# Kernel optimization log

Measured on AMD Instinct MI355X. Metric: run time of the kernel, lower is better.

## Reference

```python
import jax, jax.numpy as jnp
import numpy as np

K = 4096   # infeatures (k)
N = 4096   # outfeatures (n)
G = 128    # quantization groupsize
M = 8192   # tokens (batch*seq)


def setup_inputs() -> dict:
    key = jax.random.key(0)
    kA, kB, kS = jax.random.split(key, 3)
    A = jax.random.normal(kA, (M, K), dtype=jnp.float32)
    # Packed int4 weights: each int32 holds 8 consecutive nibbles along k.
    B = jax.random.randint(kB, (K // 8, N), 0, 2**31 - 1, dtype=jnp.int32)
    # Per-group symmetric scales, positive and small like real quant scales.
    s = jax.random.uniform(kS, (K // G, N), dtype=jnp.float32) * 0.02 + 0.005
    return {"A": A, "B": B, "s": s}


def dequant(B, s):
    """Unpack int4 nibbles, center by 8 (symmetric zero-point), apply per-group scales.
    B: (K//8, N) int32 -> returns (K, N) float weight matrix."""
    shifts = (jnp.arange(8, dtype=jnp.int32) * 4)
    nib = (B[:, None, :] >> shifts[None, :, None]) & 0xF       # (K//8, 8, N) in [0,15]
    w = nib.reshape(B.shape[0] * 8, B.shape[1]).astype(s.dtype) - 8.0  # (K, N)
    scale = jnp.repeat(s, w.shape[0] // s.shape[0], axis=0)    # (K, N) group-broadcast
    return w * scale


def reference(A, B, s):
    # C = A @ dequant(B, s): fused int4-dequant GEMM (Marlin forward math).
    return A @ dequant(B, s)
```

## Files before the change

kernel.cpp:

```cpp
#include <hip/hip_runtime.h>
#include <hip/hip_fp16.h>


constexpr int MDIM = 8192;
constexpr int NDIM = 4096;
constexpr int KDIM = 4096;
constexpr int BM = 128;
constexpr int BN = 128;
constexpr int BK = 64;
constexpr int THREADS = 256;
constexpr int KSTEPS = KDIM / BK;
constexpr int TILE_B = BM * BK * 2;
constexpr int MT = MDIM / BM;
constexpr int NT = NDIM / BN;
constexpr size_t AH_BYTES = (size_t)MT * KSTEPS * TILE_B;
constexpr size_t WT_BYTES = (size_t)NT * KSTEPS * TILE_B;

typedef _Float16 f16x8 __attribute__((ext_vector_type(8)));
typedef float f32x4 __attribute__((ext_vector_type(4)));
typedef __attribute__((address_space(3))) unsigned int lds_u32;
typedef const __attribute__((address_space(1))) unsigned int glb_u32;

__device__ __forceinline__ unsigned int pack_dq(unsigned int q, __half2 k1032,
                                                __half2 sh) {
  __half2 h = __builtin_bit_cast(__half2, q);
  h = __hmul2(__hsub2(h, k1032), sh);
  return __builtin_bit_cast(unsigned int, h);
}

__device__ __forceinline__ unsigned int cvt2(float lo, float hi) {
  auto p = __builtin_amdgcn_cvt_pkrtz(lo, hi);
  return __builtin_bit_cast(unsigned int, p);
}


__global__ __launch_bounds__(THREADS)
void prep_a(const float* __restrict__ A, char* __restrict__ Ah) {
  const int bid = blockIdx.x;
  const int mt = bid >> 6, kt = bid & 63;
  const int t = threadIdx.x;
  const int ar = t >> 3;
  const int ac = t & 7;
  char* tile = Ah + (size_t)bid * TILE_B;
#pragma unroll
  for (int i = 0; i < 4; ++i) {
    const int r = ar + 32 * i;
    const float* src = A + (size_t)(mt * BM + r) * KDIM + kt * BK + ac * 8;
    const float4 v0 = *reinterpret_cast<const float4*>(src);
    const float4 v1 = *reinterpret_cast<const float4*>(src + 4);
    uint4 w;
    w.x = cvt2(v0.x, v1.x);
    w.y = cvt2(v0.y, v1.y);
    w.z = cvt2(v0.z, v1.z);
    w.w = cvt2(v0.w, v1.w);
    *reinterpret_cast<uint4*>(tile + ((r * 128 + ac * 16) ^ ((r & 7) << 4))) = w;
  }
}

__global__ __launch_bounds__(THREADS)
void prep_b(const int* __restrict__ Bq, const float* __restrict__ S,
            char* __restrict__ Wt) {
  const int bid = blockIdx.x;
  const int nt = bid >> 6, kt = bid & 63;
  const int t = threadIdx.x;
  const int kp = t >> 5;
  const int nl = (t & 31) * 4;
  char* tile = Wt + (size_t)bid * TILE_B;
  const int4 bv = *reinterpret_cast<const int4*>(
      Bq + (size_t)(kt * 8 + kp) * NDIM + nt * BN + nl);
  const float4 sv = *reinterpret_cast<const float4*>(
      S + (size_t)(kt >> 1) * NDIM + nt * BN + nl);
  const __half2 k1032 = __float2half2_rn(1032.0f);
  const int bw[4] = {bv.x, bv.y, bv.z, bv.w};
  const float sc[4] = {sv.x, sv.y, sv.z, sv.w};
#pragma unroll
  for (int j = 0; j < 4; ++j) {
    const unsigned int ub = (unsigned int)bw[j];
    const unsigned int m4 = 0x000F000Fu, e10 = 0x64006400u;
    const __half2 sh = __float2half2_rn(sc[j]);
    uint4 w;
    w.x = pack_dq((ub & m4) | e10, k1032, sh);
    w.y = pack_dq(((ub >> 4) & m4) | e10, k1032, sh);
    w.z = pack_dq(((ub >> 8) & m4) | e10, k1032, sh);
    w.w = pack_dq(((ub >> 12) & m4) | e10, k1032, sh);
    const int r = nl + j;
    *reinterpret_cast<uint4*>(tile + ((r * 128 + kp * 16) ^ ((r & 7) << 4))) = w;
  }
}


__global__ __launch_bounds__(THREADS, 3)
void gemm_f16(const char* __restrict__ Ah, const char* __restrict__ Wt,
              float* __restrict__ C) {
  __shared__ char lds[2 * TILE_B];
  char* const As = lds;
  char* const Bs = lds + TILE_B;

  const int tid  = threadIdx.x;
  const int lane = tid & 63;
  const int wave = tid >> 6;
  const int wm = (wave >> 1) * 64;
  const int wn = (wave & 1) * 64;

  const int per = gridDim.x >> 3;
  const int b   = blockIdx.x;
  const int swzb = (b & 7) * per + (b >> 3);
  const int nt  = swzb & 31;
  const int mt  = swzb >> 5;
  const char* atiles = Ah + (size_t)mt * KSTEPS * TILE_B;
  const char* btiles = Wt + (size_t)nt * KSTEPS * TILE_B;

  f32x4 acc[4][4];
#pragma unroll
  for (int i = 0; i < 4; ++i)
#pragma unroll
    for (int j = 0; j < 4; ++j)
      acc[i][j] = f32x4{0.f, 0.f, 0.f, 0.f};

  const int swzr = (lane & 7) << 4;
  const int arow = wm + (lane & 15);
  const int brow = wn + (lane & 15);
  const int kofs = (lane >> 4) << 4;
  const int so   = wave * 1024 + lane * 16;
  const int sd   = wave * 1024;

#pragma unroll 1
  for (int kt = 0; kt < KSTEPS; ++kt) {
    const char* at = atiles + (size_t)kt * TILE_B;
    const char* bt = btiles + (size_t)kt * TILE_B;
#pragma unroll
    for (int i = 0; i < 4; ++i) {
      __builtin_amdgcn_global_load_lds((glb_u32*)(at + i * 4096 + so),
                                       (lds_u32*)(As + i * 4096 + sd), 16, 0, 0);
      __builtin_amdgcn_global_load_lds((glb_u32*)(bt + i * 4096 + so),
                                       (lds_u32*)(Bs + i * 4096 + sd), 16, 0, 0);
    }
    __syncthreads();

#pragma unroll
    for (int ks = 0; ks < 2; ++ks) {
      f16x8 af[4], bf[4];
#pragma unroll
      for (int mi = 0; mi < 4; ++mi) {
        const int o = ((arow + mi * 16) * 128 + ks * 64 + kofs) ^ swzr;
        af[mi] = *reinterpret_cast<const f16x8*>(As + o);
      }
#pragma unroll
      for (int ni = 0; ni < 4; ++ni) {
        const int o = ((brow + ni * 16) * 128 + ks * 64 + kofs) ^ swzr;
        bf[ni] = *reinterpret_cast<const f16x8*>(Bs + o);
      }
#pragma unroll
      for (int mi = 0; mi < 4; ++mi)
#pragma unroll
        for (int ni = 0; ni < 4; ++ni)
          acc[mi][ni] = __builtin_amdgcn_mfma_f32_16x16x32_f16(
              af[mi], bf[ni], acc[mi][ni], 0, 0, 0);
    }
    __syncthreads();
  }

  const int crow = (lane >> 4) << 2;
  const int ccol = lane & 15;
  const int row0 = mt * BM, col0 = nt * BN;
#pragma unroll
  for (int mi = 0; mi < 4; ++mi)
#pragma unroll
    for (int ni = 0; ni < 4; ++ni) {
      const size_t base = (size_t)(row0 + wm + mi * 16 + crow) * NDIM
                          + (size_t)(col0 + wn + ni * 16 + ccol);
#pragma unroll
      for (int r = 0; r < 4; ++r)
        C[base + (size_t)r * NDIM] = acc[mi][ni][r];
    }
}


__global__ __launch_bounds__(THREADS, 2)
void marlin_fused(const float* __restrict__ A, const int* __restrict__ Bq,
                  const float* __restrict__ S, float* __restrict__ C) {
  __shared__ char lds[2 * TILE_B];
  char* As = lds;
  char* Bs = lds + TILE_B;

  const int tid  = threadIdx.x;
  const int lane = tid & 63;
  const int wave = tid >> 6;
  const int wm = (wave >> 1) * 64;
  const int wn = (wave & 1) * 64;

  const int per = gridDim.x >> 3;
  const int b   = blockIdx.x;
  const int swz = (b & 7) * per + (b >> 3);
  const int nt  = swz & 31;
  const int mt  = swz >> 5;
  const int row0 = mt * BM;
  const int col0 = nt * BN;

  f32x4 acc[4][4];
#pragma unroll
  for (int i = 0; i < 4; ++i)
#pragma unroll
    for (int j = 0; j < 4; ++j)
      acc[i][j] = f32x4{0.f, 0.f, 0.f, 0.f};

  const int ar = tid >> 3;
  const int ac = tid & 7;
  const float* a_src = A + (size_t)(row0 + ar) * KDIM + ac * 8;
  const int a_off0 = (ar * 128 + ac * 16) ^ ((ar & 7) << 4);

  const int kp = tid >> 5;
  const int nl = (tid & 31) * 4;
  const int* b_src = Bq + (size_t)kp * NDIM + col0 + nl;
  const float* s_src = S + col0 + nl;
  int bofs[4];
#pragma unroll
  for (int j = 0; j < 4; ++j) {
    const int r = nl + j;
    bofs[j] = (r * 128 + kp * 16) ^ ((((r & 7) ^ ((r >> 3) & 3))) << 4);
  }

  const int swzr = (lane & 7) << 4;
  const int arow = wm + (lane & 15);
  const int brow = wn + (lane & 15);
  const int kofs = (lane >> 4) << 4;

  float4 av[4][2];
  int4 bv;
  float4 sv;

  auto load_tile = [&](int kt) {
#pragma unroll
    for (int i = 0; i < 4; ++i) {
      const float* src = a_src + (size_t)i * 32 * KDIM + kt * BK;
      av[i][0] = *reinterpret_cast<const float4*>(src);
      av[i][1] = *reinterpret_cast<const float4*>(src + 4);
    }
    bv = *reinterpret_cast<const int4*>(b_src + (size_t)kt * 8 * NDIM);
    sv = *reinterpret_cast<const float4*>(s_src + (size_t)(kt >> 1) * NDIM);
  };

  auto stage_tile = [&]() {
#pragma unroll
    for (int i = 0; i < 4; ++i) {
      uint4 w;
      w.x = cvt2(av[i][0].x, av[i][1].x);
      w.y = cvt2(av[i][0].y, av[i][1].y);
      w.z = cvt2(av[i][0].z, av[i][1].z);
      w.w = cvt2(av[i][0].w, av[i][1].w);
      *reinterpret_cast<uint4*>(As + a_off0 + i * 32 * 128) = w;
    }
    const __half2 k1032 = __float2half2_rn(1032.0f);
    const int bw[4] = {bv.x, bv.y, bv.z, bv.w};
    const float sc[4] = {sv.x, sv.y, sv.z, sv.w};
#pragma unroll
    for (int j = 0; j < 4; ++j) {
      const unsigned int ub = (unsigned int)bw[j];
      const unsigned int m4 = 0x000F000Fu, e10 = 0x64006400u;
      const __half2 sh = __float2half2_rn(sc[j]);
      uint4 w;
      w.x = pack_dq((ub & m4) | e10, k1032, sh);
      w.y = pack_dq(((ub >> 4) & m4) | e10, k1032, sh);
      w.z = pack_dq(((ub >> 8) & m4) | e10, k1032, sh);
      w.w = pack_dq(((ub >> 12) & m4) | e10, k1032, sh);
      *reinterpret_cast<uint4*>(Bs + bofs[j]) = w;
    }
  };

  auto compute_tile = [&]() {
#pragma unroll
    for (int ks = 0; ks < 2; ++ks) {
      f16x8 af[4], bf[4];
#pragma unroll
      for (int mi = 0; mi < 4; ++mi) {
        const int o = ((arow + mi * 16) * 128 + ks * 64 + kofs) ^ swzr;
        af[mi] = *reinterpret_cast<const f16x8*>(As + o);
      }
#pragma unroll
      for (int ni = 0; ni < 4; ++ni) {
        const int r = brow + ni * 16;
        const int o = (r * 128 + ks * 64 + kofs) ^
                      ((((r & 7) ^ ((r >> 3) & 3))) << 4);
        bf[ni] = *reinterpret_cast<const f16x8*>(Bs + o);
      }
#pragma unroll
      for (int mi = 0; mi < 4; ++mi)
#pragma unroll
        for (int ni = 0; ni < 4; ++ni)
          acc[mi][ni] = __builtin_amdgcn_mfma_f32_16x16x32_f16(
              af[mi], bf[ni], acc[mi][ni], 0, 0, 0);
    }
  };

#pragma unroll 1
  for (int kt = 0; kt < KSTEPS; ++kt) {
    load_tile(kt);
    __syncthreads();
    stage_tile();
    __syncthreads();
    compute_tile();
  }

  const int crow = (lane >> 4) << 2;
  const int ccol = lane & 15;
#pragma unroll
  for (int mi = 0; mi < 4; ++mi)
#pragma unroll
    for (int ni = 0; ni < 4; ++ni) {
      const size_t base = (size_t)(row0 + wm + mi * 16 + crow) * NDIM
                          + (size_t)(col0 + wn + ni * 16 + ccol);
#pragma unroll
      for (int r = 0; r < 4; ++r)
        C[base + (size_t)r * NDIM] = acc[mi][ni][r];
    }
}

extern "C" void kernel_launch(void* const* d_in, const int* in_sizes, int n_in,
                              void* d_out, int out_size, void* d_ws, size_t ws_size,
                              hipStream_t stream) {
  (void)in_sizes; (void)n_in; (void)out_size;
  const float* A = (const float*)d_in[0];
  const int* Bq  = (const int*)d_in[1];
  const float* S = (const float*)d_in[2];
  float* C = (float*)d_out;
  const int grid = (MDIM / BM) * (NDIM / BN);

  if (ws_size >= AH_BYTES + WT_BYTES) {
    char* Ah = (char*)d_ws;
    char* Wt = (char*)d_ws + AH_BYTES;
    prep_a<<<MT * KSTEPS, THREADS, 0, stream>>>(A, Ah);
    prep_b<<<NT * KSTEPS, THREADS, 0, stream>>>(Bq, S, Wt);
    gemm_f16<<<grid, THREADS, 0, stream>>>(Ah, Wt, C);
  } else {
    marlin_fused<<<grid, THREADS, 0, stream>>>(A, Bq, S, C);
  }
}
```

Before: 516.0 us.

## Replace GEMM with 256x256-tile, 8-wave double-buffered pipelined kernel

Replaces the 128x128 single-buffered f16 GEMM with a 256x256 block tile computed by 8 waves over 128 KB of LDS. Two stages are double-buffered, and global-to-LDS loads for the next tiles are interleaved with the MFMA quarters. Barriers, setprio and explicit vmcnt waits control the overlap. The goal is more data reuse per block and hiding load latency behind the matrix math. The cost is occupancy of one block per CU, heavy register use for the 8x4 accumulators, and fragile hand-tuned synchronization.

```diff
diff --git a/kernel.cpp b/kernel.cpp
--- a/kernel.cpp
+++ b/kernel.cpp
@@ -5,16 +5,11 @@
 constexpr int MDIM = 8192;
 constexpr int NDIM = 4096;
 constexpr int KDIM = 4096;
-constexpr int BM = 128;
-constexpr int BN = 128;
 constexpr int BK = 64;
-constexpr int THREADS = 256;
 constexpr int KSTEPS = KDIM / BK;
-constexpr int TILE_B = BM * BK * 2;
-constexpr int MT = MDIM / BM;
-constexpr int NT = NDIM / BN;
-constexpr size_t AH_BYTES = (size_t)MT * KSTEPS * TILE_B;
-constexpr size_t WT_BYTES = (size_t)NT * KSTEPS * TILE_B;
+constexpr int TILE_B = 128 * BK * 2;
+constexpr size_t AH_BYTES = (size_t)64 * KSTEPS * TILE_B;
+constexpr size_t WT_BYTES = (size_t)32 * KSTEPS * TILE_B;
 
 typedef _Float16 f16x8 __attribute__((ext_vector_type(8)));
 typedef float f32x4 __attribute__((ext_vector_type(4)));
@@ -34,7 +29,7 @@
 }
 
 
-__global__ __launch_bounds__(THREADS)
+__global__ __launch_bounds__(256)
 void prep_a(const float* __restrict__ A, char* __restrict__ Ah) {
   const int bid = blockIdx.x;
   const int mt = bid >> 6, kt = bid & 63;
@@ -45,7 +40,7 @@
 #pragma unroll
   for (int i = 0; i < 4; ++i) {
     const int r = ar + 32 * i;
-    const float* src = A + (size_t)(mt * BM + r) * KDIM + kt * BK + ac * 8;
+    const float* src = A + (size_t)(mt * 128 + r) * KDIM + kt * BK + ac * 8;
     const float4 v0 = *reinterpret_cast<const float4*>(src);
     const float4 v1 = *reinterpret_cast<const float4*>(src + 4);
     uint4 w;
@@ -57,7 +52,7 @@
   }
 }
 
-__global__ __launch_bounds__(THREADS)
+__global__ __launch_bounds__(256)
 void prep_b(const int* __restrict__ Bq, const float* __restrict__ S,
             char* __restrict__ Wt) {
   const int bid = blockIdx.x;
@@ -67,9 +62,9 @@
   const int nl = (t & 31) * 4;
   char* tile = Wt + (size_t)bid * TILE_B;
   const int4 bv = *reinterpret_cast<const int4*>(
-      Bq + (size_t)(kt * 8 + kp) * NDIM + nt * BN + nl);
+      Bq + (size_t)(kt * 8 + kp) * NDIM + nt * 128 + nl);
   const float4 sv = *reinterpret_cast<const float4*>(
-      S + (size_t)(kt >> 1) * NDIM + nt * BN + nl);
+      S + (size_t)(kt >> 1) * NDIM + nt * 128 + nl);
   const __half2 k1032 = __float2half2_rn(1032.0f);
   const int bw[4] = {bv.x, bv.y, bv.z, bv.w};
   const float sc[4] = {sv.x, sv.y, sv.z, sv.w};
@@ -89,12 +84,161 @@
 }
 
 
-__global__ __launch_bounds__(THREADS, 3)
-void gemm_f16(const char* __restrict__ Ah, const char* __restrict__ Wt,
-              float* __restrict__ C) {
+__global__ __launch_bounds__(512, 1)
+void gemm_f16_256(const char* __restrict__ Ah, const char* __restrict__ Wt,
+                  float* __restrict__ C) {
+  __shared__ char lds[131072];
+  char* const As0 = lds;
+  char* const Bs0 = lds + 32768;
+  char* const As1 = lds + 65536;
+  char* const Bs1 = lds + 98304;
+
+  const int tid  = threadIdx.x;
+  const int lane = tid & 63;
+  const int wave = tid >> 6;
+  const int wr   = wave >> 2;
+  const int wc   = wave & 3;
+
+  const int per = gridDim.x >> 3;
+  const int b   = blockIdx.x;
+  const int swzb = (b & 7) * per + (b >> 3);
+  const int ntb = swzb & 15;
+  const int mtb = swzb >> 4;
+
+  const char* aH0 = Ah + (size_t)(2 * mtb) * KSTEPS * TILE_B;
+  const char* aH1 = aH0 + (size_t)KSTEPS * TILE_B;
+  const char* bH0 = Wt + (size_t)(2 * ntb) * KSTEPS * TILE_B;
+  const char* bH1 = bH0 + (size_t)KSTEPS * TILE_B;
+
+  f32x4 acc[8][4];
+#pragma unroll
+  for (int i = 0; i < 8; ++i)
+#pragma unroll
+    for (int j = 0; j < 4; ++j)
+      acc[i][j] = f32x4{0.f, 0.f, 0.f, 0.f};
+
+  const int swzr = (lane & 7) << 4;
+  const int fr   = lane & 15;
+  const int kofs = (lane >> 4) << 4;
+  const int so   = tid * 16;
+  const int sd   = wave * 1024;
+
+  f16x8 af[4][2], bf[4][2];
+
+  auto stage_half = [&](const char* src, char* dst) {
+    __builtin_amdgcn_global_load_lds((glb_u32*)(src + so),
+                                     (lds_u32*)(dst + sd), 16, 0, 0);
+    __builtin_amdgcn_global_load_lds((glb_u32*)(src + 8192 + so),
+                                     (lds_u32*)(dst + 8192 + sd), 16, 0, 0);
+  };
+  auto rdA = [&](const char* aw, int mih) {
+#pragma unroll
+    for (int mi = 0; mi < 4; ++mi)
+#pragma unroll
+      for (int ks = 0; ks < 2; ++ks)
+        af[mi][ks] = *reinterpret_cast<const f16x8*>(
+            aw + (((mih * 64 + mi * 16 + fr) * 128 + ks * 64 + kofs) ^ swzr));
+  };
+  auto rdB = [&](const char* bw) {
+#pragma unroll
+    for (int ni = 0; ni < 4; ++ni)
+#pragma unroll
+      for (int ks = 0; ks < 2; ++ks)
+        bf[ni][ks] = *reinterpret_cast<const f16x8*>(
+            bw + ((((wc & 1) * 64 + ni * 16 + fr) * 128 + ks * 64 + kofs) ^ swzr));
+  };
+  auto mmaq = [&](int mih, int nih) {
+#pragma unroll
+    for (int mi = 0; mi < 4; ++mi)
+#pragma unroll
+      for (int ni = 0; ni < 2; ++ni)
+#pragma unroll
+        for (int ks = 0; ks < 2; ++ks)
+          acc[mih * 4 + mi][nih * 2 + ni] = __builtin_amdgcn_mfma_f32_16x16x32_f16(
+              af[mi][ks], bf[nih * 2 + ni][ks], acc[mih * 4 + mi][nih * 2 + ni],
+              0, 0, 0);
+  };
+
+  auto tile_step = [&](char* AC, char* BC, int t2, int mode) {
+    const char* aw = AC + wr * 16384;
+    const char* bw = BC + (wc >> 1) * 16384;
+    rdA(aw, 0);
+    rdB(bw);
+    __builtin_amdgcn_s_barrier();
+    __builtin_amdgcn_s_setprio(1);
+    mmaq(0, 0);
+    __builtin_amdgcn_s_setprio(0);
+    __builtin_amdgcn_s_barrier();
+    if (mode == 0) stage_half(bH0 + (size_t)t2 * TILE_B, BC);
+    __builtin_amdgcn_s_barrier();
+    __builtin_amdgcn_s_setprio(1);
+    mmaq(0, 1);
+    __builtin_amdgcn_s_setprio(0);
+    __builtin_amdgcn_s_barrier();
+    rdA(aw, 1);
+    if (mode == 0) stage_half(bH1 + (size_t)t2 * TILE_B, BC + 16384);
+    __builtin_amdgcn_s_barrier();
+    __builtin_amdgcn_s_setprio(1);
+    mmaq(1, 0);
+    __builtin_amdgcn_s_setprio(0);
+    __builtin_amdgcn_s_barrier();
+    if (mode == 0) {
+      stage_half(aH0 + (size_t)t2 * TILE_B, AC);
+      stage_half(aH1 + (size_t)t2 * TILE_B, AC + 16384);
+    }
+    __builtin_amdgcn_s_barrier();
+    __builtin_amdgcn_s_setprio(1);
+    mmaq(1, 1);
+    __builtin_amdgcn_s_setprio(0);
+    if (mode == 0) {
+      asm volatile("s_waitcnt vmcnt(8)" ::: "memory");
+      __builtin_amdgcn_sched_barrier(0);
+    } else if (mode == 1) {
+      asm volatile("s_waitcnt vmcnt(0)" ::: "memory");
+      __builtin_amdgcn_sched_barrier(0);
+    }
+    __builtin_amdgcn_s_barrier();
+  };
+
+  stage_half(aH0, As0); stage_half(aH1, As0 + 16384);
+  stage_half(bH0, Bs0); stage_half(bH1, Bs0 + 16384);
+  stage_half(aH0 + TILE_B, As1); stage_half(aH1 + TILE_B, As1 + 16384);
+  stage_half(bH0 + TILE_B, Bs1); stage_half(bH1 + TILE_B, Bs1 + 16384);
+  asm volatile("s_waitcnt vmcnt(8)" ::: "memory");
+  __builtin_amdgcn_sched_barrier(0);
+  __builtin_amdgcn_s_barrier();
+
+#pragma unroll 1
+  for (int t = 0; t < KSTEPS - 2; t += 2) {
+    tile_step(As0, Bs0, t + 2, 0);
+    tile_step(As1, Bs1, t + 3, 0);
+  }
+  tile_step(As0, Bs0, 0, 1);
+  tile_step(As1, Bs1, 0, 2);
+
+  const int crow = (lane >> 4) << 2;
+  const int ccol = lane & 15;
+  const int row0 = mtb * 256 + wr * 128;
+  const int col0 = ntb * 256 + wc * 64;
+#pragma unroll
+  for (int mi = 0; mi < 8; ++mi)
+#pragma unroll
+    for (int ni = 0; ni < 4; ++ni) {
+      const size_t base = (size_t)(row0 + mi * 16 + crow) * NDIM
+                          + (size_t)(col0 + ni * 16 + ccol);
+#pragma unroll
+      for (int r = 0; r < 4; ++r)
+        C[base + (size_t)r * NDIM] = acc[mi][ni][r];
+    }
+}
+
+
+__global__ __launch_bounds__(256, 2)
+void marlin_fused(const float* __restrict__ A, const int* __restrict__ Bq,
+                  const float* __restrict__ S, float* __restrict__ C) {
   __shared__ char lds[2 * TILE_B];
-  char* const As = lds;
-  char* const Bs = lds + TILE_B;
+  char* As = lds;
+  char* Bs = lds + TILE_B;
 
   const int tid  = threadIdx.x;
   const int lane = tid & 63;
@@ -104,98 +248,11 @@
 
   const int per = gridDim.x >> 3;
   const int b   = blockIdx.x;
-  const int swzb = (b & 7) * per + (b >> 3);
-  const int nt  = swzb & 31;
-  const int mt  = swzb >> 5;
-  const char* atiles = Ah + (size_t)mt * KSTEPS * TILE_B;
-  const char* btiles = Wt + (size_t)nt * KSTEPS * TILE_B;
-
-  f32x4 acc[4][4];
-#pragma unroll
-  for (int i = 0; i < 4; ++i)
-#pragma unroll
-    for (int j = 0; j < 4; ++j)
-      acc[i][j] = f32x4{0.f, 0.f, 0.f, 0.f};
-
-  const int swzr = (lane & 7) << 4;
-  const int arow = wm + (lane & 15);
-  const int brow = wn + (lane & 15);
-  const int kofs = (lane >> 4) << 4;
-  const int so   = wave * 1024 + lane * 16;
-  const int sd   = wave * 1024;
-
-#pragma unroll 1
-  for (int kt = 0; kt < KSTEPS; ++kt) {
-    const char* at = atiles + (size_t)kt * TILE_B;
-    const char* bt = btiles + (size_t)kt * TILE_B;
-#pragma unroll
-    for (int i = 0; i < 4; ++i) {
-      __builtin_amdgcn_global_load_lds((glb_u32*)(at + i * 4096 + so),
-                                       (lds_u32*)(As + i * 4096 + sd), 16, 0, 0);
-      __builtin_amdgcn_global_load_lds((glb_u32*)(bt + i * 4096 + so),
-                                       (lds_u32*)(Bs + i * 4096 + sd), 16, 0, 0);
-    }
-    __syncthreads();
-
-#pragma unroll
-    for (int ks = 0; ks < 2; ++ks) {
-      f16x8 af[4], bf[4];
-#pragma unroll
-      for (int mi = 0; mi < 4; ++mi) {
-        const int o = ((arow + mi * 16) * 128 + ks * 64 + kofs) ^ swzr;
-        af[mi] = *reinterpret_cast<const f16x8*>(As + o);
-      }
-#pragma unroll
-      for (int ni = 0; ni < 4; ++ni) {
-        const int o = ((brow + ni * 16) * 128 + ks * 64 + kofs) ^ swzr;
-        bf[ni] = *reinterpret_cast<const f16x8*>(Bs + o);
-      }
-#pragma unroll
-      for (int mi = 0; mi < 4; ++mi)
-#pragma unroll
-        for (int ni = 0; ni < 4; ++ni)
-          acc[mi][ni] = __builtin_amdgcn_mfma_f32_16x16x32_f16(
-              af[mi], bf[ni], acc[mi][ni], 0, 0, 0);
-    }
-    __syncthreads();
-  }
-
-  const int crow = (lane >> 4) << 2;
-  const int ccol = lane & 15;
-  const int row0 = mt * BM, col0 = nt * BN;
-#pragma unroll
-  for (int mi = 0; mi < 4; ++mi)
-#pragma unroll
-    for (int ni = 0; ni < 4; ++ni) {
-      const size_t base = (size_t)(row0 + wm + mi * 16 + crow) * NDIM
-                          + (size_t)(col0 + wn + ni * 16 + ccol);
-#pragma unroll
-      for (int r = 0; r < 4; ++r)
-        C[base + (size_t)r * NDIM] = acc[mi][ni][r];
-    }
-}
-
-
-__global__ __launch_bounds__(THREADS, 2)
-void marlin_fused(const float* __restrict__ A, const int* __restrict__ Bq,
-                  const float* __restrict__ S, float* __restrict__ C) {
-  __shared__ char lds[2 * TILE_B];
-  char* As = lds;
-  char* Bs = lds + TILE_B;
-
-  const int tid  = threadIdx.x;
-  const int lane = tid & 63;
-  const int wave = tid >> 6;
-  const int wm = (wave >> 1) * 64;
-  const int wn = (wave & 1) * 64;
-
-  const int per = gridDim.x >> 3;
-  const int b   = blockIdx.x;
   const int swz = (b & 7) * per + (b >> 3);
   const int nt  = swz & 31;
   const int mt  = swz >> 5;
-  const int row0 = mt * BM;
-  const int col0 = nt * BN;
+  const int row0 = mt * 128;
+  const int col0 = nt * 128;
 
   f32x4 acc[4][4];
 #pragma unroll
@@ -323,15 +380,14 @@
   const int* Bq  = (const int*)d_in[1];
   const float* S = (const float*)d_in[2];
   float* C = (float*)d_out;
-  const int grid = (MDIM / BM) * (NDIM / BN);
 
   if (ws_size >= AH_BYTES + WT_BYTES) {
     char* Ah = (char*)d_ws;
     char* Wt = (char*)d_ws + AH_BYTES;
-    prep_a<<<MT * KSTEPS, THREADS, 0, stream>>>(A, Ah);
-    prep_b<<<NT * KSTEPS, THREADS, 0, stream>>>(Bq, S, Wt);
-    gemm_f16<<<grid, THREADS, 0, stream>>>(Ah, Wt, C);
+    prep_a<<<64 * KSTEPS, 256, 0, stream>>>(A, Ah);
+    prep_b<<<32 * KSTEPS, 256, 0, stream>>>(Bq, S, Wt);
+    gemm_f16_256<<<(MDIM / 256) * (NDIM / 256), 512, 0, stream>>>(Ah, Wt, C);
   } else {
-    marlin_fused<<<grid, THREADS, 0, stream>>>(A, Bq, S, C);
-  }
-}
+    marlin_fused<<<2048, 256, 0, stream>>>(A, Bq, S, C);
+  }
+}
```

Result: faster. 461.2 us (-10.6%).
